# Performance work log

Measured on AMD Instinct MI355X. Metric: run time of the kernel, lower is better.

The kernel has to match this reference:

```python
import jax, jax.numpy as jnp
import numpy as np

N, E, IN, D, G, C = 100000, 3200000, 128, 512, 64, 10
EPS = 1e-5

def _bn(x, g, b):
    # training-mode BatchNorm1d: batch statistics, biased variance
    m = jnp.mean(x, axis=0)
    v = jnp.var(x, axis=0)
    return (x - m) * jax.lax.rsqrt(v + EPS) * g + b

def _prelu(x, a):
    return jnp.where(x >= 0, x, a * x)

def setup_inputs() -> dict:
    key = jax.random.key(0)
    ks = jax.random.split(key, 16)
    def w(k, shape):
        fan_in = shape[0]
        s = 1.0 / np.sqrt(fan_in)
        return jax.random.uniform(k, shape, jnp.float32, -s, s)
    inp = {
        'x': jax.random.normal(ks[0], (N, IN), jnp.float32),
        'edge_index': jax.random.randint(ks[1], (2, E), 0, N),
        'batch': jnp.sort(jax.random.randint(ks[2], (N,), 0, G)),
        'bn1_g': jnp.ones((IN,), jnp.float32), 'bn1_b': jnp.zeros((IN,), jnp.float32),
        'w0': w(ks[3], (IN, D)), 'b0': jnp.zeros((D,), jnp.float32),
        'w1': w(ks[4], (D, D)), 'bb1': jnp.zeros((D,), jnp.float32),
        'w2': w(ks[5], (D, D)), 'bb2': jnp.zeros((D,), jnp.float32),
        'w3': w(ks[6], (D, D)), 'bb3': jnp.zeros((D,), jnp.float32),
        'bn3_g': jnp.ones((D,), jnp.float32), 'bn3_b': jnp.zeros((D,), jnp.float32),
        'a3': jnp.array([0.25], jnp.float32),
        'fc1_w': w(ks[7], (D, D)), 'fc1_b': jnp.zeros((D,), jnp.float32),
        'fc2_w': w(ks[8], (D, D // 2)), 'fc2_b': jnp.zeros((D // 2,), jnp.float32),
        'fc3_w': w(ks[9], (D // 2, C)), 'fc3_b': jnp.zeros((C,), jnp.float32),
    }
    return inp

def reference(x, edge_index, batch, bn1_g, bn1_b, w0, b0, w1, bb1, w2, bb2, w3, bb3,
              bn3_g, bn3_b, a3, fc1_w, fc1_b, fc2_w, fc2_b, fc3_w, fc3_b):
    # ChebConv with K=1 reduces to a plain linear layer (T_0(L)x = x); edge_index unused.
    h = _bn(x, bn1_g, bn1_b)
    h = jax.nn.relu(h @ w0 + b0)
    for w_, b_ in ((w1, bb1), (w2, bb2), (w3, bb3)):
        h = jax.nn.relu(h @ w_ + b_)
        h = _bn(h, bn3_g, bn3_b)   # same bn3 module reused each layer
    # global_add_pool: segment-sum of node features per graph
    h = jax.ops.segment_sum(h, batch, num_segments=G)
    h = _prelu(h @ fc1_w + fc1_b, a3)
    h = jax.nn.sigmoid(h @ fc2_w + fc2_b)
    return h @ fc3_w + fc3_b
```

## Files before the change

### kernel.cpp

```cpp
#include <hip/hip_runtime.h>
#include <math.h>

#define NN 100000
#define INF 128
#define DD  512
#define GG  64
#define CC  10

typedef __bf16 bf16;
typedef __bf16 bf16x8 __attribute__((ext_vector_type(8)));
typedef __bf16 bf16x4 __attribute__((ext_vector_type(4)));
typedef float  f32x4  __attribute__((ext_vector_type(4)));
typedef unsigned int u32x4 __attribute__((ext_vector_type(4)));

#define NRB ((NN + 127) / 128)
#define CPX ((NRB + 7) / 8)
#define GEMM_GRID (8 * CPX * 4)

__device__ __forceinline__ void gld16(const bf16* g, bf16* l) {
    __builtin_amdgcn_global_load_lds(
        (const __attribute__((address_space(1))) unsigned int*)g,
        (__attribute__((address_space(3))) unsigned int*)l, 16, 0, 0);
}

__device__ __forceinline__ float bn_s(const float* stats, const float* gamma,
                                      int K, int k) {
    const float invN = 1.0f / (float)NN;
    float mean = stats[k] * invN;
    float var  = stats[K + k] * invN - mean * mean;
    return gamma[k] * rsqrtf(var + 1e-5f);
}
__device__ __forceinline__ float bn_t(const float* stats, const float* gamma,
                                      const float* beta, int K, int k) {
    const float invN = 1.0f / (float)NN;
    float mean = stats[k] * invN;
    float var  = stats[K + k] * invN - mean * mean;
    float sv   = gamma[k] * rsqrtf(var + 1e-5f);
    return beta[k] - mean * sv;
}


__global__ void zero_k(float* __restrict__ p, int n) {
    int i = blockIdx.x * blockDim.x + threadIdx.x;
    if (i < n) p[i] = 0.0f;
}

__global__ void bounds_k(const int* __restrict__ batch, int* __restrict__ starts) {
    int g = threadIdx.x;
    if (g <= GG) {
        int lo = 0, hi = NN;
        while (lo < hi) {
            int mid = (lo + hi) >> 1;
            if (batch[mid] < g) lo = mid + 1; else hi = mid;
        }
        starts[g] = lo;
    }
}

__global__ __launch_bounds__(256)
void colstats_cvt(const float* __restrict__ x, bf16* __restrict__ xb,
                  float* __restrict__ stats) {
    __shared__ float rs[4][128], rq[4][128];
    int t = threadIdx.x;
    int w = t >> 6, l = t & 63;
    int rg = t >> 5;
    int cq = t & 31;
    float s0 = 0, s1 = 0, s2 = 0, s3 = 0, q0 = 0, q1 = 0, q2 = 0, q3 = 0;
    for (int row = blockIdx.x * 8 + rg; row < NN; row += gridDim.x * 8) {
        float4 v = *(const float4*)&x[(size_t)row * INF + cq * 4];
        bf16x4 o; o[0] = (bf16)v.x; o[1] = (bf16)v.y; o[2] = (bf16)v.z; o[3] = (bf16)v.w;
        *(bf16x4*)&xb[(size_t)row * INF + cq * 4] = o;
        s0 += v.x; q0 += v.x * v.x;
        s1 += v.y; q1 += v.y * v.y;
        s2 += v.z; q2 += v.z * v.z;
        s3 += v.w; q3 += v.w * v.w;
    }
    s0 += __shfl_xor(s0, 32); s1 += __shfl_xor(s1, 32);
    s2 += __shfl_xor(s2, 32); s3 += __shfl_xor(s3, 32);
    q0 += __shfl_xor(q0, 32); q1 += __shfl_xor(q1, 32);
    q2 += __shfl_xor(q2, 32); q3 += __shfl_xor(q3, 32);
    if (l < 32) {
        rs[w][cq * 4 + 0] = s0; rs[w][cq * 4 + 1] = s1;
        rs[w][cq * 4 + 2] = s2; rs[w][cq * 4 + 3] = s3;
        rq[w][cq * 4 + 0] = q0; rq[w][cq * 4 + 1] = q1;
        rq[w][cq * 4 + 2] = q2; rq[w][cq * 4 + 3] = q3;
    }
    __syncthreads();
    if (t < 128) {
        atomicAdd(&stats[t],       rs[0][t] + rs[1][t] + rs[2][t] + rs[3][t]);
        atomicAdd(&stats[INF + t], rq[0][t] + rq[1][t] + rq[2][t] + rq[3][t]);
    }
}

__global__ __launch_bounds__(256)
void fold_wt(const float* __restrict__ stats, const float* __restrict__ gamma,
             const float* __restrict__ W, bf16* __restrict__ Wt, int K) {
    __shared__ float tile[64][68];
    __shared__ float sarr[64];
    int j0 = blockIdx.x * 64, k0 = blockIdx.y * 64;
    int t = threadIdx.x;
    if (t < 64) sarr[t] = stats ? bn_s(stats, gamma, K, k0 + t) : 1.0f;
    int kk = t >> 2, jq = t & 3;
#pragma unroll
    for (int i = 0; i < 4; i++) {
        float4 v = *(const float4*)&W[(size_t)(k0 + kk) * DD + j0 + jq * 16 + i * 4];
        *(float4*)&tile[kk][jq * 16 + i * 4] = v;
    }
    __syncthreads();
    int jj = t >> 2, kq = t & 3;
    bf16 ov[16];
#pragma unroll
    for (int i = 0; i < 16; i++)
        ov[i] = (bf16)(tile[kq * 16 + i][jj] * sarr[kq * 16 + i]);
    bf16* dst = &Wt[(size_t)(j0 + jj) * K + k0 + kq * 16];
    *(u32x4*)dst       = *(u32x4*)&ov[0];
    *(u32x4*)(dst + 8) = *(u32x4*)&ov[8];
}

__global__ __launch_bounds__(256)
void fold_b(const float* __restrict__ stats, const float* __restrict__ gamma,
            const float* __restrict__ beta, const float* __restrict__ W,
            const float* __restrict__ b, float* __restrict__ bp, int K) {
    __shared__ float red[4][64];
    __shared__ float tt[DD];
    int t = threadIdx.x;
    for (int k = t; k < K; k += 256) tt[k] = bn_t(stats, gamma, beta, K, k);
    __syncthreads();
    int jj = t & 63, kr = t >> 6;
    int j = blockIdx.x * 64 + jj;
    float acc = 0.f;
    for (int k = kr; k < K; k += 4)
        acc += tt[k] * W[(size_t)k * DD + j];
    red[kr][jj] = acc;
    __syncthreads();
    if (kr == 0) bp[j] = b[j] + red[0][jj] + red[1][jj] + red[2][jj] + red[3][jj];
}

template <int K, int MODE>
__global__ __launch_bounds__(256, 4)
void gemm_mfma(const bf16* __restrict__ A, const bf16* __restrict__ Wt,
               const float* __restrict__ bias, bf16* __restrict__ H, int M,
               float* __restrict__ stats, const int* __restrict__ batch,
               float* __restrict__ R) {
    const int id  = blockIdx.x;
    const int xcd = id & 7;
    const int jj  = id >> 3;
    const int yb  = xcd * CPX + (jj >> 2);
    if (yb >= NRB) return;
    const int col0 = (jj & 3) * 128;
    const int row0 = yb * 128;

    __shared__ bf16 smem[18432];
    bf16* As = smem;
    bf16* Bs = smem + 8192;
    const int t  = threadIdx.x;
    const int l  = t & 63;
    const int w  = t >> 6;
    const int wr = w >> 1, wc = w & 1;

    const int srow = w * 8 + (l >> 3);
    const int sslt = l & 7;

    f32x4 acc[4][4];
#pragma unroll
    for (int m = 0; m < 4; m++)
#pragma unroll
        for (int n = 0; n < 4; n++) acc[m][n] = (f32x4){0.f, 0.f, 0.f, 0.f};

#pragma unroll 1
    for (int k0 = 0; k0 < K; k0 += 64) {
#pragma unroll
        for (int c = 0; c < 4; c++) {
            int r  = c * 32 + srow;
            int sg = sslt ^ (r & 7);
            int ga = row0 + r; if (ga >= M) ga = M - 1;
            gld16(A  + (size_t)ga * K + k0 + sg * 8,
                  (bf16*)((char*)As + c * 4096 + w * 1024));
            gld16(Wt + (size_t)(col0 + r) * K + k0 + sg * 8,
                  (bf16*)((char*)Bs + c * 4096 + w * 1024));
        }
        __syncthreads();
#pragma unroll
        for (int ks = 0; ks < 2; ks++) {
            bf16x8 af[4], bfr[4];
#pragma unroll
            for (int m = 0; m < 4; m++) {
                int r = wr * 64 + m * 16 + (l & 15);
                af[m] = *(const bf16x8*)((const char*)As + r * 128 +
                        ((((ks << 2) + (l >> 4)) ^ (r & 7)) << 4));
            }
#pragma unroll
            for (int n = 0; n < 4; n++) {
                int r = wc * 64 + n * 16 + (l & 15);
                bfr[n] = *(const bf16x8*)((const char*)Bs + r * 128 +
                         ((((ks << 2) + (l >> 4)) ^ (r & 7)) << 4));
            }
#pragma unroll
            for (int m = 0; m < 4; m++)
#pragma unroll
                for (int n = 0; n < 4; n++)
                    acc[m][n] = __builtin_amdgcn_mfma_f32_16x16x32_bf16(af[m], bfr[n], acc[m][n], 0, 0, 0);
        }
        __syncthreads();
    }

    float csumA[4], csqA[4];

    if (MODE <= 1) {
        bf16* ct = smem;
#pragma unroll
        for (int n = 0; n < 4; n++) {
            int lc = wc * 64 + n * 16 + (l & 15);
            float bv = bias[col0 + lc];
            float cs = 0.f, cq = 0.f;
#pragma unroll
            for (int m = 0; m < 4; m++) {
#pragma unroll
                for (int q = 0; q < 4; q++) {
                    int lr = wr * 64 + m * 16 + (l >> 4) * 4 + q;
                    float v = acc[m][n][q] + bv;
                    v = v > 0.f ? v : 0.f;
                    ct[lr * 136 + lc] = (bf16)v;
                    if (MODE == 1 && row0 + lr < M) { cs += v; cq += v * v; }
                }
            }
            csumA[n] = cs; csqA[n] = cq;
        }
        __syncthreads();
        {
            const char* cts = (const char*)ct;
            char* Hc = (char*)H;
#pragma unroll
            for (int i = 0; i < 8; i++) {
                int fo = i * 4096 + t * 16;
                int r  = fo >> 8;
                int cb = fo & 255;
                if (row0 + r < M)
                    *(u32x4*)(Hc + ((size_t)(row0 + r) * (DD * 2) + (size_t)col0 * 2 + cb)) =
                        *(const u32x4*)(cts + r * 272 + cb);
            }
        }
    } else {
        int gid[4][4];
#pragma unroll
        for (int m = 0; m < 4; m++)
#pragma unroll
            for (int q = 0; q < 4; q++) {
                int grow = row0 + wr * 64 + m * 16 + (l >> 4) * 4 + q;
                gid[m][q] = (grow < M) ? batch[grow] : -1;
            }
#pragma unroll
        for (int n = 0; n < 4; n++) {
            int col = col0 + wc * 64 + n * 16 + (l & 15);
            float bv = bias[col];
            float cs = 0.f, cq = 0.f;
            float ps = 0.f; int gc = -1;
#pragma unroll
            for (int m = 0; m < 4; m++) {
#pragma unroll
                for (int q = 0; q < 4; q++) {
                    int g = gid[m][q];
                    if (g >= 0) {
                        float v = acc[m][n][q] + bv;
                        v = v > 0.f ? v : 0.f;
                        cs += v; cq += v * v;
                        if (g != gc) {
                            if (gc >= 0) atomicAdd(&R[(size_t)gc * DD + col], ps);
                            ps = 0.f; gc = g;
                        }
                        ps += v;
                    }
                }
            }
            if (gc >= 0) atomicAdd(&R[(size_t)gc * DD + col], ps);
            csumA[n] = cs; csqA[n] = cq;
        }
    }

    if (MODE >= 1) {
#pragma unroll
        for (int n = 0; n < 4; n++) {
            float cs = csumA[n], cq = csqA[n];
            cs += __shfl_xor(cs, 16); cs += __shfl_xor(cs, 32);
            cq += __shfl_xor(cq, 16); cq += __shfl_xor(cq, 32);
            if ((l >> 4) == 0) {
                int col = col0 + wc * 64 + n * 16 + l;
                atomicAdd(&stats[col], cs);
                atomicAdd(&stats[DD + col], cq);
            }
        }
    }
}

__global__ __launch_bounds__(512)
void pool_fin(const float* __restrict__ R, const int* __restrict__ starts,
              const float* __restrict__ stats, const float* __restrict__ gamma,
              const float* __restrict__ beta, float* __restrict__ P) {
    int g = blockIdx.x, j = threadIdx.x;
    float sv = bn_s(stats, gamma, DD, j);
    float tv = bn_t(stats, gamma, beta, DD, j);
    float cnt = (float)(starts[g + 1] - starts[g]);
    P[g * DD + j] = R[(size_t)g * DD + j] * sv + cnt * tv;
}

__global__ __launch_bounds__(256)
void head_k(const float* __restrict__ P,
            const float* __restrict__ fc1_w, const float* __restrict__ fc1_b,
            const float* __restrict__ fc2_w, const float* __restrict__ fc2_b,
            const float* __restrict__ fc3_w, const float* __restrict__ fc3_b,
            const float* __restrict__ a3, float* __restrict__ out) {
    __shared__ float p[DD], y1[DD], y2[DD / 2];
    int g = blockIdx.x, t = threadIdx.x;
    p[t]       = P[g * DD + t];
    p[t + 256] = P[g * DD + t + 256];
    __syncthreads();
    float alpha = a3[0];

    float acc0 = fc1_b[t], acc1 = fc1_b[t + 256];
    for (int k = 0; k < DD; k++) {
        float pv = p[k];
        acc0 = fmaf(pv, fc1_w[(size_t)k * DD + t], acc0);
        acc1 = fmaf(pv, fc1_w[(size_t)k * DD + t + 256], acc1);
    }
    y1[t]       = acc0 >= 0.f ? acc0 : alpha * acc0;
    y1[t + 256] = acc1 >= 0.f ? acc1 : alpha * acc1;
    __syncthreads();

    float acc = fc2_b[t];
    for (int k = 0; k < DD; k++) acc = fmaf(y1[k], fc2_w[(size_t)k * (DD / 2) + t], acc);
    y2[t] = 1.0f / (1.0f + expf(-acc));
    __syncthreads();

    if (t < CC) {
        float a = fc3_b[t];
        for (int k = 0; k < DD / 2; k++) a = fmaf(y2[k], fc3_w[(size_t)k * CC + t], a);
        out[g * CC + t] = a;
    }
}

extern "C" void kernel_launch(void* const* d_in, const int* in_sizes, int n_in,
                              void* d_out, int out_size, void* d_ws, size_t ws_size,
                              hipStream_t stream) {
    const float* x     = (const float*)d_in[0];
    const int*   batch = (const int*)d_in[2];
    const float* bn1_g = (const float*)d_in[3];
    const float* bn1_b = (const float*)d_in[4];
    const float* w0    = (const float*)d_in[5];
    const float* b0    = (const float*)d_in[6];
    const float* w1    = (const float*)d_in[7];
    const float* bb1   = (const float*)d_in[8];
    const float* w2    = (const float*)d_in[9];
    const float* bb2   = (const float*)d_in[10];
    const float* w3    = (const float*)d_in[11];
    const float* bb3   = (const float*)d_in[12];
    const float* bn3_g = (const float*)d_in[13];
    const float* bn3_b = (const float*)d_in[14];
    const float* a3    = (const float*)d_in[15];
    const float* fc1_w = (const float*)d_in[16];
    const float* fc1_b = (const float*)d_in[17];
    const float* fc2_w = (const float*)d_in[18];
    const float* fc2_b = (const float*)d_in[19];
    const float* fc3_w = (const float*)d_in[20];
    const float* fc3_b = (const float*)d_in[21];
    float* out = (float*)d_out;

    char* base = (char*)d_ws;
    const size_t HBYTES = (size_t)NN * DD * 2;
    bf16* Ha = (bf16*)base;
    bf16* Hb = (bf16*)(base + HBYTES);
    bf16* Xb = Hb;
    bf16* Wt = (bf16*)(base + 2 * HBYTES);
    float* f = (float*)(base + 2 * HBYTES + 524288);
    size_t off = 0;
    float* stats  = f + off; off += 3328;
    float* R      = f + off; off += (size_t)GG * DD;
    float* statsX = stats;
    float* stats2 = stats + 256;
    float* stats3 = stats + 1280;
    float* stats4 = stats + 2304;
    float* b0p = f + off; off += 512;
    float* bp  = f + off; off += 512;
    float* P   = f + off; off += (size_t)GG * DD;
    int*   starts = (int*)(f + off); off += 128;

    (void)in_sizes; (void)n_in; (void)out_size; (void)ws_size;

    const int kZeroCount = 3328 + GG * DD;

    zero_k<<<(kZeroCount + 255) / 256, 256, 0, stream>>>(stats, kZeroCount);
    bounds_k<<<1, 128, 0, stream>>>(batch, starts);

    colstats_cvt<<<256, 256, 0, stream>>>(x, Xb, statsX);
    fold_wt<<<dim3(8, INF / 64), 256, 0, stream>>>(statsX, bn1_g, w0, Wt, INF);
    fold_b<<<8, 256, 0, stream>>>(statsX, bn1_g, bn1_b, w0, b0, b0p, INF);
    gemm_mfma<INF, 0><<<GEMM_GRID, 256, 0, stream>>>(Xb, Wt, b0p, Ha, NN, nullptr, nullptr, nullptr);

    fold_wt<<<dim3(8, DD / 64), 256, 0, stream>>>(nullptr, nullptr, w1, Wt, DD);
    gemm_mfma<DD, 1><<<GEMM_GRID, 256, 0, stream>>>(Ha, Wt, bb1, Hb, NN, stats2, nullptr, nullptr);

    fold_wt<<<dim3(8, DD / 64), 256, 0, stream>>>(stats2, bn3_g, w2, Wt, DD);
    fold_b<<<8, 256, 0, stream>>>(stats2, bn3_g, bn3_b, w2, bb2, bp, DD);
    gemm_mfma<DD, 1><<<GEMM_GRID, 256, 0, stream>>>(Hb, Wt, bp, Ha, NN, stats3, nullptr, nullptr);

    fold_wt<<<dim3(8, DD / 64), 256, 0, stream>>>(stats3, bn3_g, w3, Wt, DD);
    fold_b<<<8, 256, 0, stream>>>(stats3, bn3_g, bn3_b, w3, bb3, bp, DD);
    gemm_mfma<DD, 2><<<GEMM_GRID, 256, 0, stream>>>(Ha, Wt, bp, nullptr, NN, stats4, batch, R);

    pool_fin<<<GG, 512, 0, stream>>>(R, starts, stats4, bn3_g, bn3_b, P);
    head_k<<<GG, 256, 0, stream>>>(P, fc1_w, fc1_b, fc2_w, fc2_b, fc3_w, fc3_b, a3, out);
}
```

Before: 603.6 us.

## Double-buffer GEMM LDS tiles and drop XCD-aware block swizzle

The MFMA GEMM now stages the next K-tile into a second LDS buffer while computing on the current one, leaving one barrier per iteration instead of two, so global loads can overlap with compute. LDS use roughly doubles to 64KB per block and the launch bound drops to 2 blocks per CU, which reduces occupancy. The launch also replaces the XCD-aware 1D swizzled grid with a plain 2D grid (4 column tiles × row blocks). That may lose L2 locality of A rows across XCDs.

```diff
diff --git a/kernel.cpp b/kernel.cpp
--- a/kernel.cpp
+++ b/kernel.cpp
@@ -14,8 +14,6 @@
 typedef unsigned int u32x4 __attribute__((ext_vector_type(4)));
 
 #define NRB ((NN + 127) / 128)
-#define CPX ((NRB + 7) / 8)
-#define GEMM_GRID (8 * CPX * 4)
 
 __device__ __forceinline__ void gld16(const bf16* g, bf16* l) {
     __builtin_amdgcn_global_load_lds(
@@ -137,26 +135,18 @@
 }
 
 template <int K, int MODE>
-__global__ __launch_bounds__(256, 4)
+__global__ __launch_bounds__(256, 2)
 void gemm_mfma(const bf16* __restrict__ A, const bf16* __restrict__ Wt,
                const float* __restrict__ bias, bf16* __restrict__ H, int M,
                float* __restrict__ stats, const int* __restrict__ batch,
                float* __restrict__ R) {
-    const int id  = blockIdx.x;
-    const int xcd = id & 7;
-    const int jj  = id >> 3;
-    const int yb  = xcd * CPX + (jj >> 2);
-    if (yb >= NRB) return;
-    const int col0 = (jj & 3) * 128;
-    const int row0 = yb * 128;
-
-    __shared__ bf16 smem[18432];
-    bf16* As = smem;
-    bf16* Bs = smem + 8192;
+    __shared__ bf16 smem[32768];
     const int t  = threadIdx.x;
     const int l  = t & 63;
     const int w  = t >> 6;
     const int wr = w >> 1, wc = w & 1;
+    const int col0 = blockIdx.x * 128;
+    const int row0 = blockIdx.y * 128;
 
     const int srow = w * 8 + (l >> 3);
     const int sslt = l & 7;
@@ -167,8 +157,9 @@
 #pragma unroll
         for (int n = 0; n < 4; n++) acc[m][n] = (f32x4){0.f, 0.f, 0.f, 0.f};
 
-#pragma unroll 1
-    for (int k0 = 0; k0 < K; k0 += 64) {
+    auto stage = [&](int b, int k0) {
+        bf16* As = smem + b * 16384;
+        bf16* Bs = As + 8192;
 #pragma unroll
         for (int c = 0; c < 4; c++) {
             int r  = c * 32 + srow;
@@ -179,7 +170,11 @@
             gld16(Wt + (size_t)(col0 + r) * K + k0 + sg * 8,
                   (bf16*)((char*)Bs + c * 4096 + w * 1024));
         }
-        __syncthreads();
+    };
+
+    auto compute = [&](int b) {
+        const bf16* As = smem + b * 16384;
+        const bf16* Bs = As + 8192;
 #pragma unroll
         for (int ks = 0; ks < 2; ks++) {
             bf16x8 af[4], bfr[4];
@@ -201,8 +196,20 @@
                 for (int n = 0; n < 4; n++)
                     acc[m][n] = __builtin_amdgcn_mfma_f32_16x16x32_bf16(af[m], bfr[n], acc[m][n], 0, 0, 0);
         }
+    };
+
+    int cur = 0;
+    stage(0, 0);
+    __syncthreads();
+#pragma unroll 1
+    for (int k0 = 64; k0 < K; k0 += 64) {
+        stage(cur ^ 1, k0);
+        compute(cur);
         __syncthreads();
-    }
+        cur ^= 1;
+    }
+    compute(cur);
+    __syncthreads();
 
     float csumA[4], csqA[4];
 
@@ -385,6 +392,7 @@
 
     (void)in_sizes; (void)n_in; (void)out_size; (void)ws_size;
 
+    const dim3 ggrid(4, NRB);
     const int kZeroCount = 3328 + GG * DD;
 
     zero_k<<<(kZeroCount + 255) / 256, 256, 0, stream>>>(stats, kZeroCount);
@@ -393,18 +401,18 @@
     colstats_cvt<<<256, 256, 0, stream>>>(x, Xb, statsX);
     fold_wt<<<dim3(8, INF / 64), 256, 0, stream>>>(statsX, bn1_g, w0, Wt, INF);
     fold_b<<<8, 256, 0, stream>>>(statsX, bn1_g, bn1_b, w0, b0, b0p, INF);
-    gemm_mfma<INF, 0><<<GEMM_GRID, 256, 0, stream>>>(Xb, Wt, b0p, Ha, NN, nullptr, nullptr, nullptr);
+    gemm_mfma<INF, 0><<<ggrid, 256, 0, stream>>>(Xb, Wt, b0p, Ha, NN, nullptr, nullptr, nullptr);
 
     fold_wt<<<dim3(8, DD / 64), 256, 0, stream>>>(nullptr, nullptr, w1, Wt, DD);
-    gemm_mfma<DD, 1><<<GEMM_GRID, 256, 0, stream>>>(Ha, Wt, bb1, Hb, NN, stats2, nullptr, nullptr);
+    gemm_mfma<DD, 1><<<ggrid, 256, 0, stream>>>(Ha, Wt, bb1, Hb, NN, stats2, nullptr, nullptr);
 
     fold_wt<<<dim3(8, DD / 64), 256, 0, stream>>>(stats2, bn3_g, w2, Wt, DD);
     fold_b<<<8, 256, 0, stream>>>(stats2, bn3_g, bn3_b, w2, bb2, bp, DD);
-    gemm_mfma<DD, 1><<<GEMM_GRID, 256, 0, stream>>>(Hb, Wt, bp, Ha, NN, stats3, nullptr, nullptr);
+    gemm_mfma<DD, 1><<<ggrid, 256, 0, stream>>>(Hb, Wt, bp, Ha, NN, stats3, nullptr, nullptr);
 
     fold_wt<<<dim3(8, DD / 64), 256, 0, stream>>>(stats3, bn3_g, w3, Wt, DD);
     fold_b<<<8, 256, 0, stream>>>(stats3, bn3_g, bn3_b, w3, bb3, bp, DD);
-    gemm_mfma<DD, 2><<<GEMM_GRID, 256, 0, stream>>>(Ha, Wt, bp, nullptr, NN, stats4, batch, R);
+    gemm_mfma<DD, 2><<<ggrid, 256, 0, stream>>>(Ha, Wt, bp, nullptr, NN, stats4, batch, R);
 
     pool_fin<<<GG, 512, 0, stream>>>(R, starts, stats4, bn3_g, bn3_b, P);
     head_k<<<GG, 256, 0, stream>>>(P, fc1_w, fc1_b, fc2_w, fc2_b, fc3_w, fc3_b, a3, out);
```

Result: slower. 661.3 us (+9.6%).
